# Kernel tuning notes

Hardware: AMD Instinct MI355X
Metric: run time of the kernel (lower is better)

## Reference

```python
import jax, jax.numpy as jnp
import numpy as np

B, S, D = 2, 2048, 1024
H = 16
DH = D // H
FFN = 4096
EPS = 1e-5
SCALE = 1.0 / np.sqrt(DH).astype(np.float32)


def layer_norm(x, g, b):
    mu = jnp.mean(x, axis=-1, keepdims=True)
    var = jnp.mean(jnp.square(x - mu), axis=-1, keepdims=True)
    return (x - mu) * jax.lax.rsqrt(var + EPS) * g + b


def setup_inputs() -> dict:
    key = jax.random.key(0)
    ks = jax.random.split(key, 12)
    std = 0.02
    return {
        "x": jax.random.normal(ks[0], (B, S, D), dtype=jnp.float32),
        "mask": jax.random.randint(ks[1], (B, S), 0, 2, dtype=jnp.int32),
        "w_qkv": jax.random.normal(ks[2], (D, 3 * D), dtype=jnp.float32) * std,
        "w_out": jax.random.normal(ks[3], (D, D), dtype=jnp.float32) * std,
        "b_out": jnp.zeros((D,), dtype=jnp.float32),
        "g1": jnp.ones((D,), dtype=jnp.float32),
        "be1": jnp.zeros((D,), dtype=jnp.float32),
        "g2": jnp.ones((D,), dtype=jnp.float32),
        "be2": jnp.zeros((D,), dtype=jnp.float32),
        "w1": jax.random.normal(ks[4], (D, FFN), dtype=jnp.float32) * std,
        "b1": jnp.zeros((FFN,), dtype=jnp.float32),
        "w2": jax.random.normal(ks[5], (FFN, D), dtype=jnp.float32) * std,
        "b2": jnp.zeros((D,), dtype=jnp.float32),
    }


def reference(x, mask, w_qkv, w_out, b_out, g1, be1, g2, be2, w1, b1, w2, b2):
    # --- pre-norm self-attention ---
    h = layer_norm(x, g1, be1)                              # [B,S,D]
    qkv = (h @ w_qkv).reshape(B, S, 3, H, DH)               # [B,S,3,H,Dh]
    q, k, v = [jnp.transpose(qkv[:, :, i], (0, 2, 1, 3)) for i in range(3)]  # [B,H,S,Dh]
    scores = jnp.einsum("bhqd,bhkd->bhqk", q, k) * SCALE    # [B,H,S,S]
    key_mask = (mask != 0)[:, None, None, :]                # [B,1,1,S]
    scores = jnp.where(key_mask, scores, -1e9)
    attn = jax.nn.softmax(scores, axis=-1)
    out = jnp.einsum("bhqk,bhkd->bhqd", attn, v)            # [B,H,S,Dh]
    out = jnp.transpose(out, (0, 2, 1, 3)).reshape(B, S, D)
    x = x + (out @ w_out + b_out)
    # --- pre-norm FFN ---
    h2 = layer_norm(x, g2, be2)
    ffn = jax.nn.relu(h2 @ w1 + b1) @ w2 + b2
    return x + ffn
```

## Files before the change

### kernel.cpp

```cpp
#include <hip/hip_runtime.h>

typedef unsigned short u16;
typedef __bf16 bf16x8 __attribute__((ext_vector_type(8)));
typedef float f32x4 __attribute__((ext_vector_type(4)));

typedef __attribute__((address_space(1))) const void* as1cv;
typedef __attribute__((address_space(3))) void* as3v;

__device__ __forceinline__ u16 f2bf(float f) {
  union { float f; unsigned u; } v;
  v.f = f;
  unsigned r = (v.u + 0x7fffu + ((v.u >> 16) & 1u)) >> 16;
  return (u16)r;
}

__device__ __forceinline__ unsigned cvtpk(float lo, float hi) {
  unsigned r;
  asm("v_cvt_pk_bf16_f32 %0, %1, %2" : "=v"(r) : "v"(lo), "v"(hi));
  return r;
}

__device__ __forceinline__ void gload16(const void* g, void* l) {
  __builtin_amdgcn_global_load_lds((as1cv)g, (as3v)l, 16, 0, 0);
}

__global__ __launch_bounds__(256)
void ln_kernel(const float* __restrict__ x, const float* __restrict__ g,
               const float* __restrict__ be, u16* __restrict__ out) {
  __shared__ float red[8];
  const int row = blockIdx.x;
  const int tid = threadIdx.x;
  const float4 v = ((const float4*)(x + (size_t)row * 1024))[tid];
  float s = v.x + v.y + v.z + v.w;
#pragma unroll
  for (int off = 1; off < 64; off <<= 1) s += __shfl_xor(s, off, 64);
  const int wv = tid >> 6, lane = tid & 63;
  if (lane == 0) red[wv] = s;
  __syncthreads();
  s = red[0] + red[1] + red[2] + red[3];
  const float mu = s * (1.0f / 1024.0f);
  const float d0 = v.x - mu, d1 = v.y - mu, d2 = v.z - mu, d3 = v.w - mu;
  float q = d0 * d0 + d1 * d1 + d2 * d2 + d3 * d3;
#pragma unroll
  for (int off = 1; off < 64; off <<= 1) q += __shfl_xor(q, off, 64);
  if (lane == 0) red[4 + wv] = q;
  __syncthreads();
  q = red[4] + red[5] + red[6] + red[7];
  const float inv = rsqrtf(q * (1.0f / 1024.0f) + 1e-5f);
  const float4 gv = ((const float4*)g)[tid];
  const float4 bv = ((const float4*)be)[tid];
  unsigned p0 = (unsigned)f2bf(d0 * inv * gv.x + bv.x) |
                ((unsigned)f2bf(d1 * inv * gv.y + bv.y) << 16);
  unsigned p1 = (unsigned)f2bf(d2 * inv * gv.z + bv.z) |
                ((unsigned)f2bf(d3 * inv * gv.w + bv.w) << 16);
  uint2 o; o.x = p0; o.y = p1;
  *(uint2*)(out + (size_t)row * 1024 + tid * 4) = o;
}

__global__ __launch_bounds__(256)
void transpose_all(const float* __restrict__ i0, u16* __restrict__ o0,
                   const float* __restrict__ i1, u16* __restrict__ o1,
                   const float* __restrict__ i2, u16* __restrict__ o2,
                   const float* __restrict__ i3, u16* __restrict__ o3) {
  __shared__ float t[32][33];
  int id = blockIdx.x;
  const float* in; u16* out; int K, N, nx;
  if (id < 3072)      { in = i0; out = o0; K = 1024; N = 3072; nx = 96; }
  else if (id < 4096) { id -= 3072; in = i1; out = o1; K = 1024; N = 1024; nx = 32; }
  else if (id < 8192) { id -= 4096; in = i2; out = o2; K = 1024; N = 4096; nx = 128; }
  else                { id -= 8192; in = i3; out = o3; K = 4096; N = 1024; nx = 32; }
  const int n0 = (id % nx) * 32, k0 = (id / nx) * 32;
  const int tx = threadIdx.x & 31, ty = threadIdx.x >> 5;
  for (int r = ty; r < 32; r += 8)
    t[r][tx] = in[(size_t)(k0 + r) * N + n0 + tx];
  __syncthreads();
  for (int r = ty; r < 32; r += 8)
    out[(size_t)(n0 + r) * K + k0 + tx] = f2bf(t[tx][r]);
}

template<int BIAS, int RELU, int RES, int MODE, int NSPLIT>
__global__ __launch_bounds__(256, 2)
void gemm_bt(const u16* __restrict__ A, const u16* __restrict__ Bt,
             const float* __restrict__ bias, const float* __restrict__ res,
             void* __restrict__ C, u16* __restrict__ vt,
             int M, int N, int K, int kChunk) {
  __shared__ u16 As[4][4096];
  __shared__ u16 Bs[4][4096];
  const int tid = threadIdx.x;
  const int wv = tid >> 6, lane = tid & 63;
  const int z = (NSPLIT > 1) ? (int)(blockIdx.x % NSPLIT) : 0;
  const int bm = (int)(blockIdx.x / NSPLIT) * 128;
  const int bn = blockIdx.y * 128;
  const int wr = wv >> 1, wc = wv & 1;
  const int l16 = lane & 15, lh = lane >> 4;

  const int ssk = ((lane & 3) ^ ((lane >> 3) & 3)) << 3;
  const int rdk = (lh ^ ((l16 >> 1) & 3)) << 3;

  f32x4 acc[4][4] = {};

  const int kb = z * kChunk;
  const u16* Ag = A + (size_t)(bm + wv * 16 + (lane >> 2)) * K + kb + ssk;
  const u16* Bg = Bt + (size_t)(bn + wv * 16 + (lane >> 2)) * K + kb + ssk;

#define STG_A(buf, ko)  do { \
    gload16(Ag + (ko), &As[buf][wv * 512]); \
    gload16(Ag + (size_t)64 * K + (ko), &As[buf][2048 + wv * 512]); } while (0)
#define STG_B(buf, ko)  do { \
    gload16(Bg + (ko), &Bs[buf][wv * 512]); \
    gload16(Bg + (size_t)64 * K + (ko), &Bs[buf][2048 + wv * 512]); } while (0)

  const int nst = kChunk >> 5;
  STG_A(0, 0); STG_B(0, 0);
  if (nst > 1) { STG_A(1, 32); STG_B(1, 32); }
  if (nst > 2) { STG_A(2, 64); STG_B(2, 64); }

  for (int t = 0; t < nst; ++t) {
    const int cur = t & 3;
    const int rem = nst - t;
    if (rem >= 3)      asm volatile("s_waitcnt vmcnt(8)" ::: "memory");
    else if (rem == 2) asm volatile("s_waitcnt vmcnt(4)" ::: "memory");
    else               asm volatile("s_waitcnt vmcnt(0)" ::: "memory");
    __builtin_amdgcn_s_barrier();
    asm volatile("" ::: "memory");
    const int nxb = (t + 3) & 3;
    bf16x8 af[4], bfv[4];
#pragma unroll
    for (int i = 0; i < 4; i++)
      af[i] = *(const bf16x8*)&As[cur][(wr * 64 + i * 16 + l16) * 32 + rdk];
#pragma unroll
    for (int j = 0; j < 2; j++)
      bfv[j] = *(const bf16x8*)&Bs[cur][(wc * 64 + j * 16 + l16) * 32 + rdk];
    if (t + 3 < nst) STG_A(nxb, (t + 3) * 32);
    __builtin_amdgcn_s_setprio(1);
#pragma unroll
    for (int i = 0; i < 4; i++)
#pragma unroll
      for (int j = 0; j < 2; j++)
        acc[i][j] = __builtin_amdgcn_mfma_f32_16x16x32_bf16(af[i], bfv[j], acc[i][j], 0, 0, 0);
    __builtin_amdgcn_s_setprio(0);
#pragma unroll
    for (int j = 2; j < 4; j++)
      bfv[j] = *(const bf16x8*)&Bs[cur][(wc * 64 + j * 16 + l16) * 32 + rdk];
    if (t + 3 < nst) STG_B(nxb, (t + 3) * 32);
    __builtin_amdgcn_s_setprio(1);
#pragma unroll
    for (int i = 0; i < 4; i++)
#pragma unroll
      for (int j = 2; j < 4; j++)
        acc[i][j] = __builtin_amdgcn_mfma_f32_16x16x32_bf16(af[i], bfv[j], acc[i][j], 0, 0, 0);
    __builtin_amdgcn_s_setprio(0);
  }
#undef STG_A
#undef STG_B

#pragma unroll
  for (int i = 0; i < 4; i++) {
#pragma unroll
    for (int j = 0; j < 4; j++) {
      const int col = bn + wc * 64 + j * 16 + l16;
      const float bv = (BIAS && z == 0) ? bias[col] : 0.0f;
      if (MODE == 3 && bn >= 2048) {
        const int cc = col - 2048, h = cc >> 6, d = cc & 63;
        const int row0 = bm + wr * 64 + i * 16 + (lane >> 4) * 4;
        const int bb = row0 >> 11, kv0 = row0 & 2047;
        const int p0 = (kv0 & 32) | (((kv0 >> 2) & 3) << 3) | (((kv0 >> 4) & 1) << 2);
        uint2 o;
        o.x = (unsigned)f2bf(acc[i][j][0]) | ((unsigned)f2bf(acc[i][j][1]) << 16);
        o.y = (unsigned)f2bf(acc[i][j][2]) | ((unsigned)f2bf(acc[i][j][3]) << 16);
        *(uint2*)(vt + ((size_t)(bb * 16 + h) * 64 + d) * 2048 + (kv0 & ~63) + p0) = o;
      } else {
#pragma unroll
        for (int r = 0; r < 4; r++) {
          const int row = bm + wr * 64 + i * 16 + (lane >> 4) * 4 + r;
          float v = acc[i][j][r] + bv;
          if (RELU) v = fmaxf(v, 0.0f);
          if (RES) v += res[(size_t)row * N + col];
          if (MODE == 2)       atomicAdd((float*)C + (size_t)row * N + col, v);
          else if (MODE == 0)  ((float*)C)[(size_t)row * N + col] = v;
          else                 ((u16*)C)[(size_t)row * N + col] = f2bf(v);
        }
      }
    }
  }
}

template<int BIAS, int RELU, int MODE>
__global__ __launch_bounds__(512, 2)
void gemm256(const u16* __restrict__ A, const u16* __restrict__ Bt,
             const float* __restrict__ bias, u16* __restrict__ C,
             u16* __restrict__ vt, int M, int N, int K) {
  __shared__ u16 As[2][16384];
  __shared__ u16 Bs[2][16384];
  const int tid = threadIdx.x;
  const int wv = tid >> 6, lane = tid & 63;
  const int l16 = lane & 15, lh = lane >> 4;
  const int wm = wv >> 2, wn = wv & 3;
  const int bm = blockIdx.x * 256, bn = blockIdx.y * 256;

  const int koff = ((lane & 7) ^ ((lane >> 3) & 7)) << 3;
  const int ka0 = ((lh ^ (l16 & 7)) << 3);
  const int ka1 = (((4 + lh) ^ (l16 & 7)) << 3);

  f32x4 acc[8][4] = {};

  const u16* Ag = A + (size_t)(bm + wv * 8 + (lane >> 3)) * K + koff;
  const u16* Bg = Bt + (size_t)(bn + wv * 8 + (lane >> 3)) * K + koff;

#define STAGE256(buf, ko)                                                  \
  do {                                                                     \
    _Pragma("unroll")                                                      \
    for (int j = 0; j < 4; ++j) {                                          \
      gload16(Ag + (size_t)(j * 64) * K + (ko), &As[buf][j * 4096 + wv * 512]); \
      gload16(Bg + (size_t)(j * 64) * K + (ko), &Bs[buf][j * 4096 + wv * 512]); \
    }                                                                      \
  } while (0)

  const int nt = K >> 6;
  STAGE256(0, 0);
  if (nt > 1) STAGE256(1, 64);

  for (int t = 0; t < nt; ++t) {
    const int cur = t & 1;
    if (t + 1 < nt) asm volatile("s_waitcnt vmcnt(8)" ::: "memory");
    else            asm volatile("s_waitcnt vmcnt(0)" ::: "memory");
    __builtin_amdgcn_s_barrier();
    asm volatile("" ::: "memory");
#pragma unroll
    for (int kk = 0; kk < 2; ++kk) {
      const int ko = kk ? ka1 : ka0;
      bf16x8 af[8], bfv[4];
#pragma unroll
      for (int i = 0; i < 8; ++i)
        af[i] = *(const bf16x8*)&As[cur][(wm * 128 + i * 16 + l16) * 64 + ko];
#pragma unroll
      for (int n = 0; n < 4; ++n)
        bfv[n] = *(const bf16x8*)&Bs[cur][(wn * 64 + n * 16 + l16) * 64 + ko];
      __builtin_amdgcn_s_setprio(1);
#pragma unroll
      for (int i = 0; i < 8; ++i)
#pragma unroll
        for (int n = 0; n < 4; ++n)
          acc[i][n] = __builtin_amdgcn_mfma_f32_16x16x32_bf16(af[i], bfv[n], acc[i][n], 0, 0, 0);
      __builtin_amdgcn_s_setprio(0);
    }
    asm volatile("" ::: "memory");
    __builtin_amdgcn_s_barrier();
    asm volatile("" ::: "memory");
    if (t + 2 < nt) STAGE256(cur, (t + 2) * 64);
  }
#undef STAGE256

#pragma unroll
  for (int i = 0; i < 8; ++i)
#pragma unroll
    for (int n = 0; n < 4; ++n) {
      const int col = bn + wn * 64 + n * 16 + l16;
      const float bv = BIAS ? bias[col] : 0.0f;
      if (MODE == 3 && bn >= 2048) {
        const int cc = col - 2048, h = cc >> 6, d = cc & 63;
        const int row0 = bm + wm * 128 + i * 16 + lh * 4;
        const int bb = row0 >> 11, kv0 = row0 & 2047;
        const int p0 = (kv0 & 32) | (((kv0 >> 2) & 3) << 3) | (((kv0 >> 4) & 1) << 2);
        uint2 o;
        o.x = (unsigned)f2bf(acc[i][n][0]) | ((unsigned)f2bf(acc[i][n][1]) << 16);
        o.y = (unsigned)f2bf(acc[i][n][2]) | ((unsigned)f2bf(acc[i][n][3]) << 16);
        *(uint2*)(vt + ((size_t)(bb * 16 + h) * 64 + d) * 2048 + (kv0 & ~63) + p0) = o;
      } else {
#pragma unroll
        for (int r = 0; r < 4; ++r) {
          const int row = bm + wm * 128 + i * 16 + lh * 4 + r;
          float v = acc[i][n][r] + bv;
          if (RELU) v = fmaxf(v, 0.0f);
          C[(size_t)row * N + col] = f2bf(v);
        }
      }
    }
}

__global__ __launch_bounds__(256, 4)
void attn3(const u16* __restrict__ qkv, const u16* __restrict__ vT,
           const int* __restrict__ mask, u16* __restrict__ aout) {
  __shared__ u16 KsS[2][4096];
  __shared__ u16 VsS[2][4096];
  __shared__ float mbL[2048];

  const int tid = threadIdx.x;
  const int wv = tid >> 6, lane = tid & 63;
  const int l16 = lane & 15, lh = lane >> 4;
  const int bh = blockIdx.x, b = bh >> 4, h = bh & 15;
  const int q0 = blockIdx.y * 64 + wv * 16;

  {
    const int4* srcm = (const int4*)(mask + b * 2048);
    float4* dstm = (float4*)mbL;
#pragma unroll
    for (int u = 0; u < 2; ++u) {
      const int4 mv = srcm[tid + u * 256];
      float4 f;
      f.x = mv.x ? 0.f : -1.4426950408889634e9f;
      f.y = mv.y ? 0.f : -1.4426950408889634e9f;
      f.z = mv.z ? 0.f : -1.4426950408889634e9f;
      f.w = mv.w ? 0.f : -1.4426950408889634e9f;
      dstm[tid + u * 256] = f;
    }
  }

  bf16x8 qf[2];
#pragma unroll
  for (int c = 0; c < 2; ++c)
    qf[c] = *(const bf16x8*)(qkv + (size_t)(b * 2048 + q0 + l16) * 3072 + h * 64 + c * 32 + 8 * lh);

  const int rs = (l16 & 7) << 4;
  const int koff0 = ((16 * lh) ^ rs) >> 1;
  const int koff1 = ((64 + 16 * lh) ^ rs) >> 1;
  const int voff0 = koff0, voff1 = koff1;

  const int rl0 = wv * 8 + (lane >> 3);
  const int rl1 = 32 + wv * 8 + (lane >> 3);
  const int glog = (lane & 7) ^ ((lane >> 3) & 7);
  const u16* kg0 = qkv + (size_t)(b * 2048 + rl0) * 3072 + 1024 + h * 64 + 8 * glog;
  const u16* kg1 = qkv + (size_t)(b * 2048 + rl1) * 3072 + 1024 + h * 64 + 8 * glog;
  const u16* vg0 = vT + ((size_t)bh * 64 + rl0) * 2048 + 8 * glog;
  const u16* vg1 = vT + ((size_t)bh * 64 + rl1) * 2048 + 8 * glog;

  gload16(kg0, &KsS[0][wv * 512]);
  gload16(kg1, &KsS[0][2048 + wv * 512]);
  gload16(vg0, &VsS[0][wv * 512]);
  gload16(vg1, &VsS[0][2048 + wv * 512]);
  kg0 += 64 * 3072; kg1 += 64 * 3072; vg0 += 64; vg1 += 64;

  const float CL2 = 0.125f * 1.4426950408889634f;
  float lacc = 0.f;
  f32x4 oT[4] = {};

  for (int t = 0; t < 32; ++t) {
    asm volatile("s_waitcnt vmcnt(0)" ::: "memory");
    __syncthreads();
    const int cur = t & 1;
    if (t + 1 < 32) {
      const int nx = cur ^ 1;
      gload16(kg0, &KsS[nx][wv * 512]);
      gload16(kg1, &KsS[nx][2048 + wv * 512]);
      gload16(vg0, &VsS[nx][wv * 512]);
      gload16(vg1, &VsS[nx][2048 + wv * 512]);
      kg0 += 64 * 3072; kg1 += 64 * 3072; vg0 += 64; vg1 += 64;
    }

    const u16* Kb = &KsS[cur][0];
    const u16* Vb = &VsS[cur][0];

    f32x4 mbc[4];
#pragma unroll
    for (int n = 0; n < 4; ++n)
      mbc[n] = *(const f32x4*)&mbL[t * 64 + n * 16 + 4 * lh];

    f32x4 s[4] = {};
    __builtin_amdgcn_s_setprio(1);
#pragma unroll
    for (int c = 0; c < 2; ++c) {
      const int ko = c ? koff1 : koff0;
      bf16x8 kf[4];
#pragma unroll
      for (int n = 0; n < 4; ++n)
        kf[n] = *(const bf16x8*)(Kb + (n * 16 + l16) * 64 + ko);
#pragma unroll
      for (int n = 0; n < 4; ++n)
        s[n] = __builtin_amdgcn_mfma_f32_16x16x32_bf16(kf[n], qf[c], s[n], 0, 0, 0);
    }
    __builtin_amdgcn_s_setprio(0);

#pragma unroll
    for (int n = 0; n < 4; ++n)
#pragma unroll
      for (int j = 0; j < 4; ++j) {
        const float p = __builtin_exp2f(fmaf(s[n][j], CL2, mbc[n][j]));
        s[n][j] = p;
        lacc += p;
      }

    union U8 { unsigned u[4]; bf16x8 v; };
    U8 pa[2];
#pragma unroll
    for (int u = 0; u < 2; ++u) {
      pa[u].u[0] = cvtpk(s[2 * u][0], s[2 * u][1]);
      pa[u].u[1] = cvtpk(s[2 * u][2], s[2 * u][3]);
      pa[u].u[2] = cvtpk(s[2 * u + 1][0], s[2 * u + 1][1]);
      pa[u].u[3] = cvtpk(s[2 * u + 1][2], s[2 * u + 1][3]);
    }

    __builtin_amdgcn_s_setprio(1);
#pragma unroll
    for (int u = 0; u < 2; ++u) {
      const int vo = u ? voff1 : voff0;
#pragma unroll
      for (int D = 0; D < 4; ++D) {
        const bf16x8 va = *(const bf16x8*)(Vb + (D * 16 + l16) * 64 + vo);
        oT[D] = __builtin_amdgcn_mfma_f32_16x16x32_bf16(va, pa[u].v, oT[D], 0, 0, 0);
      }
    }
    __builtin_amdgcn_s_setprio(0);
  }

  lacc += __shfl_xor(lacc, 16, 64);
  lacc += __shfl_xor(lacc, 32, 64);
  const float rr = 1.0f / lacc;
#pragma unroll
  for (int D = 0; D < 4; ++D) {
    uint2 o;
    o.x = cvtpk(oT[D][0] * rr, oT[D][1] * rr);
    o.y = cvtpk(oT[D][2] * rr, oT[D][3] * rr);
    *(uint2*)(aout + (size_t)(b * 2048 + q0 + l16) * 1024 + h * 64 + D * 16 + 4 * lh) = o;
  }
}

extern "C" void kernel_launch(void* const* d_in, const int* in_sizes, int n_in,
                              void* d_out, int out_size, void* d_ws, size_t ws_size,
                              hipStream_t stream) {
  (void)in_sizes; (void)n_in; (void)out_size; (void)ws_size;
  const float* x     = (const float*)d_in[0];
  const int*   mask  = (const int*)d_in[1];
  const float* w_qkv = (const float*)d_in[2];
  const float* w_out = (const float*)d_in[3];
  const float* b_out = (const float*)d_in[4];
  const float* g1    = (const float*)d_in[5];
  const float* be1   = (const float*)d_in[6];
  const float* g2    = (const float*)d_in[7];
  const float* be2   = (const float*)d_in[8];
  const float* w1    = (const float*)d_in[9];
  const float* b1    = (const float*)d_in[10];
  const float* w2    = (const float*)d_in[11];
  const float* b2    = (const float*)d_in[12];
  float* out = (float*)d_out;

  char* ws = (char*)d_ws;
  u16* hA    = (u16*)(ws);
  u16* wqkvT = (u16*)(ws + 8388608);
  u16* woutT = (u16*)(ws + 14680064);
  u16* w1T   = (u16*)(ws + 16777216);
  u16* w2T   = (u16*)(ws + 25165824);
  u16* qkv   = (u16*)(ws + 33554432);
  u16* ffn1  = (u16*)(ws + 33554432);
  u16* vTb   = (u16*)(ws + 67108864);
  u16* aout  = (u16*)(ws + 75497472);

  ln_kernel<<<4096, 256, 0, stream>>>(x, g1, be1, hA);
  transpose_all<<<12288, 256, 0, stream>>>(w_qkv, wqkvT, w_out, woutT, w1, w1T, w2, w2T);
  gemm256<0, 0, 3><<<dim3(16, 12), 512, 0, stream>>>(hA, wqkvT, nullptr, qkv, vTb, 4096, 3072, 1024);
  attn3<<<dim3(32, 32), 256, 0, stream>>>(qkv, vTb, mask, aout);
  gemm_bt<1, 0, 1, 0, 1><<<dim3(32, 8), 256, 0, stream>>>(aout, woutT, b_out, x, out, nullptr, 4096, 1024, 1024, 1024);
  ln_kernel<<<4096, 256, 0, stream>>>(out, g2, be2, hA);
  gemm256<1, 1, 1><<<dim3(16, 16), 512, 0, stream>>>(hA, w1T, b1, ffn1, nullptr, 4096, 4096, 1024);
  gemm_bt<1, 0, 0, 2, 2><<<dim3(64, 8), 256, 0, stream>>>(ffn1, w2T, b2, nullptr, out, nullptr, 4096, 1024, 4096, 2048);
}
```

Baseline: 251.1 us.

## Load V fragments directly from global and compute softmax row-sum via MFMA

The attention kernel stops staging V tiles through shared memory and instead loads each wave's V^T fragments straight from global memory into registers every iteration, which halves shared-memory use and the async-copy traffic. The softmax denominator is now computed with an extra MFMA against a vector of bf16 ones rather than scalar adds and cross-lane shuffles. Each wave now reads V independently, so global/L2 traffic rises and load latency sits on the critical path right after the barrier. The denominator now uses bf16-rounded probabilities, which matches what feeds the PV product.

```diff
diff --git a/kernel.cpp b/kernel.cpp
--- a/kernel.cpp
+++ b/kernel.cpp
@@ -282,7 +282,6 @@
 void attn3(const u16* __restrict__ qkv, const u16* __restrict__ vT,
            const int* __restrict__ mask, u16* __restrict__ aout) {
   __shared__ u16 KsS[2][4096];
-  __shared__ u16 VsS[2][4096];
   __shared__ float mbL[2048];
 
   const int tid = threadIdx.x;
@@ -314,41 +313,46 @@
   const int rs = (l16 & 7) << 4;
   const int koff0 = ((16 * lh) ^ rs) >> 1;
   const int koff1 = ((64 + 16 * lh) ^ rs) >> 1;
-  const int voff0 = koff0, voff1 = koff1;
 
   const int rl0 = wv * 8 + (lane >> 3);
   const int rl1 = 32 + wv * 8 + (lane >> 3);
   const int glog = (lane & 7) ^ ((lane >> 3) & 7);
   const u16* kg0 = qkv + (size_t)(b * 2048 + rl0) * 3072 + 1024 + h * 64 + 8 * glog;
   const u16* kg1 = qkv + (size_t)(b * 2048 + rl1) * 3072 + 1024 + h * 64 + 8 * glog;
-  const u16* vg0 = vT + ((size_t)bh * 64 + rl0) * 2048 + 8 * glog;
-  const u16* vg1 = vT + ((size_t)bh * 64 + rl1) * 2048 + 8 * glog;
+  const u16* vg = vT + (size_t)bh * 131072 + (size_t)l16 * 2048 + lh * 8;
 
   gload16(kg0, &KsS[0][wv * 512]);
   gload16(kg1, &KsS[0][2048 + wv * 512]);
-  gload16(vg0, &VsS[0][wv * 512]);
-  gload16(vg1, &VsS[0][2048 + wv * 512]);
-  kg0 += 64 * 3072; kg1 += 64 * 3072; vg0 += 64; vg1 += 64;
+  kg0 += 64 * 3072; kg1 += 64 * 3072;
 
   const float CL2 = 0.125f * 1.4426950408889634f;
-  float lacc = 0.f;
+  f32x4 lsum = {};
   f32x4 oT[4] = {};
+  union U8 { unsigned u[4]; bf16x8 v; };
+  U8 onesu;
+  onesu.u[0] = onesu.u[1] = onesu.u[2] = onesu.u[3] = 0x3F803F80u;
+  const bf16x8 ones = onesu.v;
 
   for (int t = 0; t < 32; ++t) {
     asm volatile("s_waitcnt vmcnt(0)" ::: "memory");
     __syncthreads();
     const int cur = t & 1;
+
+    bf16x8 va[2][4];
+#pragma unroll
+    for (int u = 0; u < 2; ++u)
+#pragma unroll
+      for (int D = 0; D < 4; ++D)
+        va[u][D] = *(const bf16x8*)(vg + (size_t)(D * 16) * 2048 + t * 64 + u * 32);
+
     if (t + 1 < 32) {
       const int nx = cur ^ 1;
       gload16(kg0, &KsS[nx][wv * 512]);
       gload16(kg1, &KsS[nx][2048 + wv * 512]);
-      gload16(vg0, &VsS[nx][wv * 512]);
-      gload16(vg1, &VsS[nx][2048 + wv * 512]);
-      kg0 += 64 * 3072; kg1 += 64 * 3072; vg0 += 64; vg1 += 64;
+      kg0 += 64 * 3072; kg1 += 64 * 3072;
     }
 
     const u16* Kb = &KsS[cur][0];
-    const u16* Vb = &VsS[cur][0];
 
     f32x4 mbc[4];
 #pragma unroll
@@ -373,13 +377,9 @@
 #pragma unroll
     for (int n = 0; n < 4; ++n)
 #pragma unroll
-      for (int j = 0; j < 4; ++j) {
-        const float p = __builtin_exp2f(fmaf(s[n][j], CL2, mbc[n][j]));
-        s[n][j] = p;
-        lacc += p;
-      }
-
-    union U8 { unsigned u[4]; bf16x8 v; };
+      for (int j = 0; j < 4; ++j)
+        s[n][j] = __builtin_exp2f(fmaf(s[n][j], CL2, mbc[n][j]));
+
     U8 pa[2];
 #pragma unroll
     for (int u = 0; u < 2; ++u) {
@@ -392,19 +392,15 @@
     __builtin_amdgcn_s_setprio(1);
 #pragma unroll
     for (int u = 0; u < 2; ++u) {
-      const int vo = u ? voff1 : voff0;
-#pragma unroll
-      for (int D = 0; D < 4; ++D) {
-        const bf16x8 va = *(const bf16x8*)(Vb + (D * 16 + l16) * 64 + vo);
-        oT[D] = __builtin_amdgcn_mfma_f32_16x16x32_bf16(va, pa[u].v, oT[D], 0, 0, 0);
-      }
+      lsum = __builtin_amdgcn_mfma_f32_16x16x32_bf16(ones, pa[u].v, lsum, 0, 0, 0);
+#pragma unroll
+      for (int D = 0; D < 4; ++D)
+        oT[D] = __builtin_amdgcn_mfma_f32_16x16x32_bf16(va[u][D], pa[u].v, oT[D], 0, 0, 0);
     }
     __builtin_amdgcn_s_setprio(0);
   }
 
-  lacc += __shfl_xor(lacc, 16, 64);
-  lacc += __shfl_xor(lacc, 32, 64);
-  const float rr = 1.0f / lacc;
+  const float rr = 1.0f / lsum[0];
 #pragma unroll
   for (int D = 0; D < 4; ++D) {
     uint2 o;
```

After: 314.8 us. 1.25x slower.
